# Performance work log

Measured on AMD Instinct MI355X. Metric: run time of the kernel, lower is better.

The kernel has to match this reference:

```python
import jax, jax.numpy as jnp
import numpy as np

N_NODES = 50000
N_EDGES = 1_600_000
HID = 64
BN_EPS = 1e-5


def setup_inputs() -> dict:
    key = jax.random.key(0)
    ks = jax.random.split(key, 16)
    x = jax.random.normal(ks[0], (N_NODES, 1), dtype=jnp.float32)
    edge_index = jax.random.randint(ks[1], (2, N_EDGES), 0, N_NODES, dtype=jnp.int32)
    s = 1.0 / np.sqrt(HID)
    # layer 1: 1 -> 64 -> 64
    w1a = jax.random.normal(ks[2], (1, HID), dtype=jnp.float32)
    b1a = jnp.zeros((HID,), jnp.float32)
    w2a = jax.random.normal(ks[3], (HID, HID), dtype=jnp.float32) * s
    b2a = jnp.zeros((HID,), jnp.float32)
    # layers 2-4 stacked: 64 -> 64 -> 64
    w1s = jax.random.normal(ks[4], (3, HID, HID), dtype=jnp.float32) * s
    b1s = jnp.zeros((3, HID), jnp.float32)
    w2s = jax.random.normal(ks[5], (3, HID, HID), dtype=jnp.float32) * s
    b2s = jnp.zeros((3, HID), jnp.float32)
    eps = jnp.zeros((4,), jnp.float32)  # train_eps=True, init 0
    gammas = jnp.ones((4, HID), jnp.float32)
    betas = jnp.zeros((4, HID), jnp.float32)
    fc_w = jax.random.normal(ks[6], (HID, 1), dtype=jnp.float32) * s
    fc_b = jnp.zeros((1,), jnp.float32)
    return {"x": x, "edge_index": edge_index, "w1a": w1a, "b1a": b1a,
            "w2a": w2a, "b2a": b2a, "w1s": w1s, "b1s": b1s, "w2s": w2s,
            "b2s": b2s, "eps": eps, "gammas": gammas, "betas": betas,
            "fc_w": fc_w, "fc_b": fc_b}


def _gin(h, src, dst, e, w1, b1, w2, b2):
    # sum_{j in N(i)} h_j  (messages from src, aggregated at dst)
    agg = jax.ops.segment_sum(h[src], dst, num_segments=N_NODES)
    z = (1.0 + e) * h + agg
    return jax.nn.relu(z @ w1 + b1) @ w2 + b2


def _bn(h, g, b):
    # BatchNorm1d, training mode: biased batch statistics over nodes
    mu = jnp.mean(h, axis=0)
    var = jnp.mean((h - mu) ** 2, axis=0)
    return (h - mu) * jax.lax.rsqrt(var + BN_EPS) * g + b


def reference(x, edge_index, w1a, b1a, w2a, b2a, w1s, b1s, w2s, b2s,
              eps, gammas, betas, fc_w, fc_b):
    src, dst = edge_index[0], edge_index[1]
    h = _bn(jax.nn.relu(_gin(x, src, dst, eps[0], w1a, b1a, w2a, b2a)),
            gammas[0], betas[0])
    for i in range(3):
        h = _bn(jax.nn.relu(_gin(h, src, dst, eps[i + 1],
                                 w1s[i], b1s[i], w2s[i], b2s[i])),
                gammas[i + 1], betas[i + 1])
    return h @ fc_w + fc_b
```

## Files before the change

kernel.cpp:

```cpp
#include <hip/hip_runtime.h>

#define HID 64
#define BN_EPS 1e-5f
#define WINSH 8
#define WINSZ 256
#define B1 256
#define PIT 72

typedef short bf16x8 __attribute__((ext_vector_type(8)));
typedef float f32x4 __attribute__((ext_vector_type(4)));

__device__ __forceinline__ unsigned short f2b(float f) {
    unsigned int u = __float_as_uint(f);
    u = (u + 0x7FFF + ((u >> 16) & 1)) >> 16;
    return (unsigned short)u;
}
__device__ __forceinline__ float b2f(unsigned short h) {
    return __uint_as_float(((unsigned int)h) << 16);
}
__device__ __forceinline__ f32x4 mfma_bf16(bf16x8 a, bf16x8 b, f32x4 c) {
    return __builtin_amdgcn_mfma_f32_16x16x32_bf16(a, b, c, 0, 0, 0);
}

__global__ __launch_bounds__(256) void p1_count_kernel(const int* __restrict__ dst,
                                                       int* __restrict__ cnt,
                                                       int E, int nw, int chunk) {
    __shared__ int c[256];
    int tid = threadIdx.x, b = blockIdx.x;
    c[tid] = 0;
    __syncthreads();
    int lo = b * chunk;
    int hi = lo + chunk; if (hi > E) hi = E;
    for (int e = lo + tid; e < hi; e += 256) atomicAdd(&c[dst[e] >> WINSH], 1);
    __syncthreads();
    if (tid < nw) cnt[tid * B1 + b] = c[tid];
}

__global__ __launch_bounds__(256) void scan_a_kernel(const int* __restrict__ in,
                                                     int* __restrict__ partial,
                                                     int* __restrict__ blocksum, int n) {
    __shared__ int sums[256];
    int tid = threadIdx.x;
    int i = blockIdx.x * 256 + tid;
    int v = (i < n) ? in[i] : 0;
    sums[tid] = v;
    __syncthreads();
    for (int off = 1; off < 256; off <<= 1) {
        int t = (tid >= off) ? sums[tid - off] : 0;
        __syncthreads();
        sums[tid] += t;
        __syncthreads();
    }
    if (i < n) partial[i] = sums[tid] - v;
    if (tid == 255) blocksum[blockIdx.x] = sums[255];
}

__global__ __launch_bounds__(256) void scan_b_kernel(const int* __restrict__ blocksum,
                                                     int* __restrict__ blockoff, int nb) {
    __shared__ int s[256];
    __shared__ int carry;
    int tid = threadIdx.x;
    if (tid == 0) carry = 0;
    __syncthreads();
    for (int base = 0; base < nb; base += 256) {
        int i = base + tid;
        int v = (i < nb) ? blocksum[i] : 0;
        s[tid] = v;
        __syncthreads();
        for (int off = 1; off < 256; off <<= 1) {
            int t = (tid >= off) ? s[tid - off] : 0;
            __syncthreads();
            s[tid] += t;
            __syncthreads();
        }
        if (i < nb) blockoff[i] = carry + s[tid] - v;
        __syncthreads();
        if (tid == 0) carry += s[255];
        __syncthreads();
    }
}

__global__ __launch_bounds__(256) void scan_c_kernel(const int* __restrict__ partial,
                                                     const int* __restrict__ blockoff,
                                                     int* __restrict__ outp, int n) {
    int i = blockIdx.x * 256 + threadIdx.x;
    if (i < n) outp[i] = partial[i] + blockoff[blockIdx.x];
}

__global__ __launch_bounds__(256) void p3_bucket_kernel(const int* __restrict__ src,
                                                        const int* __restrict__ dst,
                                                        const int* __restrict__ coff,
                                                        int* __restrict__ ebuf,
                                                        int E, int nw, int chunk) {
    __shared__ int cur[256];
    int tid = threadIdx.x, b = blockIdx.x;
    if (tid < nw) cur[tid] = coff[tid * B1 + b];
    __syncthreads();
    int lo = b * chunk;
    int hi = lo + chunk; if (hi > E) hi = E;
    for (int e = lo + tid; e < hi; e += 256) {
        int d = dst[e];
        int w = d >> WINSH;
        int pos = atomicAdd(&cur[w], 1);
        ebuf[pos] = src[e] | ((d & (WINSZ - 1)) << 24);
    }
}

__global__ __launch_bounds__(256) void p4_fine_kernel(const int* __restrict__ ebuf,
                                                      const int* __restrict__ coff,
                                                      int* __restrict__ csr_src,
                                                      int* __restrict__ rowptr,
                                                      int* __restrict__ deg,
                                                      int E, int n, int nw) {
    __shared__ int fcnt[256];
    __shared__ int foff[256];
    int tid = threadIdx.x, w = blockIdx.x;
    int lo = coff[w * B1];
    int hi = (w + 1 < nw) ? coff[(w + 1) * B1] : E;
    fcnt[tid] = 0;
    __syncthreads();
    for (int e = lo + tid; e < hi; e += 256) atomicAdd(&fcnt[(unsigned)ebuf[e] >> 24], 1);
    __syncthreads();
    int v = fcnt[tid];
    foff[tid] = v;
    __syncthreads();
    for (int off = 1; off < 256; off <<= 1) {
        int t = (tid >= off) ? foff[tid - off] : 0;
        __syncthreads();
        foff[tid] += t;
        __syncthreads();
    }
    int myoff = lo + foff[tid] - v;
    int node = w * WINSZ + tid;
    if (node < n) { rowptr[node] = myoff; deg[node] = v; }
    __syncthreads();
    fcnt[tid] = myoff;
    __syncthreads();
    for (int e = lo + tid; e < hi; e += 256) {
        int p = ebuf[e];
        int pos = atomicAdd(&fcnt[(unsigned)p >> 24], 1);
        csr_src[pos] = p & 0xFFFFFF;
    }
}

__global__ __launch_bounds__(256) void wprep_kernel(const float* __restrict__ w2a,
                                                    const float* __restrict__ w1s,
                                                    const float* __restrict__ w2s,
                                                    unsigned short* __restrict__ whi,
                                                    unsigned short* __restrict__ wlo) {
    int b = blockIdx.x;
    const float* srcm = (b == 0) ? w2a : (b <= 3 ? w1s + (size_t)(b - 1) * 4096
                                                 : w2s + (size_t)(b - 4) * 4096);
    unsigned short* dh = whi + (size_t)b * 4096;
    unsigned short* dl = wlo + (size_t)b * 4096;
    for (int idx = threadIdx.x; idx < 4096; idx += 256) {
        int j = idx & 7;
        int lane = (idx >> 3) & 63;
        int ntkh = idx >> 9;
        int nt = ntkh >> 1, kh = ntkh & 1;
        int nc = nt * 16 + (lane & 15);
        int k = kh * 32 + (lane >> 4) * 8 + j;
        float v = srcm[k * 64 + nc];
        unsigned short h = f2b(v);
        dh[idx] = h;
        dl[idx] = f2b(v - b2f(h));
    }
}

__global__ __launch_bounds__(256) void gather1_kernel(const float* __restrict__ x,
                                                      const int* __restrict__ rowptr,
                                                      const int* __restrict__ deg,
                                                      const int* __restrict__ csr_src,
                                                      const float* __restrict__ eps,
                                                      float* __restrict__ zscalar, int n) {
    int node = blockIdx.x * 4 + (threadIdx.x >> 6);
    int lane = threadIdx.x & 63;
    if (node >= n) return;
    int start = __builtin_amdgcn_readfirstlane(rowptr[node]);
    int cnt   = __builtin_amdgcn_readfirstlane(deg[node]);
    float a = 0.f;
    for (int i = lane; i < cnt; i += 64) a += x[csr_src[start + i]];
    for (int off = 32; off > 0; off >>= 1) a += __shfl_xor(a, off);
    if (lane == 0) zscalar[node] = (1.0f + eps[0]) * x[node] + a;
}

__global__ __launch_bounds__(256) void gatherz_kernel(const float* __restrict__ hpre,
                                                      const float* __restrict__ bnp,
                                                      const int* __restrict__ rowptr,
                                                      const int* __restrict__ deg,
                                                      const int* __restrict__ csr_src,
                                                      const float* __restrict__ eps,
                                                      int layer,
                                                      float* __restrict__ zbuf, int n) {
    int node = blockIdx.x * 4 + (threadIdx.x >> 6);
    int lane = threadIdx.x & 63;
    if (node >= n) return;
    int start = __builtin_amdgcn_readfirstlane(rowptr[node]);
    int cnt   = __builtin_amdgcn_readfirstlane(deg[node]);
    float a0 = 0.f, a1 = 0.f, a2 = 0.f, a3 = 0.f;
    float a4 = 0.f, a5 = 0.f, a6 = 0.f, a7 = 0.f;
    int e = 0;
    for (; e + 8 <= cnt; e += 8) {
        int s0 = csr_src[start + e + 0];
        int s1 = csr_src[start + e + 1];
        int s2 = csr_src[start + e + 2];
        int s3 = csr_src[start + e + 3];
        int s4 = csr_src[start + e + 4];
        int s5 = csr_src[start + e + 5];
        int s6 = csr_src[start + e + 6];
        int s7 = csr_src[start + e + 7];
        a0 += hpre[(size_t)s0 * HID + lane];
        a1 += hpre[(size_t)s1 * HID + lane];
        a2 += hpre[(size_t)s2 * HID + lane];
        a3 += hpre[(size_t)s3 * HID + lane];
        a4 += hpre[(size_t)s4 * HID + lane];
        a5 += hpre[(size_t)s5 * HID + lane];
        a6 += hpre[(size_t)s6 * HID + lane];
        a7 += hpre[(size_t)s7 * HID + lane];
    }
    for (; e < cnt; ++e) a0 += hpre[(size_t)csr_src[start + e] * HID + lane];
    float sum = ((a0 + a1) + (a2 + a3)) + ((a4 + a5) + (a6 + a7));
    float ep = 1.0f + eps[layer];
    float sc = bnp[lane], sh = bnp[64 + lane];
    float self = hpre[(size_t)node * HID + lane];
    zbuf[(size_t)node * HID + lane] =
        fmaf(sc, fmaf(ep, self, sum), sh * (ep + (float)cnt));
}

__global__ __launch_bounds__(256) void mlp_kernel(const float* __restrict__ zin,
                                                  const float* __restrict__ zscalar,
                                                  const float* __restrict__ w1a,
                                                  const float* __restrict__ b1a,
                                                  const unsigned short* __restrict__ w1h,
                                                  const unsigned short* __restrict__ w1l,
                                                  const float* __restrict__ b1v,
                                                  const unsigned short* __restrict__ w2h,
                                                  const unsigned short* __restrict__ w2l,
                                                  const float* __restrict__ b2v,
                                                  float* __restrict__ hpre,
                                                  float* __restrict__ stats,
                                                  int n, int mode) {
    __shared__ __align__(16) unsigned short Ah[64 * PIT];
    __shared__ __align__(16) unsigned short Al[64 * PIT];
    __shared__ float ssum[64], ssq[64];

    int tid = threadIdx.x;
    int base = blockIdx.x * 64;

    if (mode) {
        for (int i = tid; i < 4096; i += 256) {
            int nn = i >> 6, k = i & 63;
            float v = zin[(size_t)(base + nn) * HID + k];
            unsigned short h = f2b(v);
            Ah[nn * PIT + k] = h;
            Al[nn * PIT + k] = f2b(v - b2f(h));
        }
    } else {
        for (int i = tid; i < 4096; i += 256) {
            int nn = i >> 6, k = i & 63;
            float zv = zscalar[base + nn];
            float v = fmaxf(fmaf(zv, w1a[k], b1a[k]), 0.f);
            unsigned short h = f2b(v);
            Ah[nn * PIT + k] = h;
            Al[nn * PIT + k] = f2b(v - b2f(h));
        }
    }
    if (tid < 64) { ssum[tid] = 0.f; ssq[tid] = 0.f; }
    __syncthreads();

    int l = tid & 63;
    int m = l & 15;
    int q = l >> 4;
    int m0 = (tid >> 6) * 16;

    const bf16x8* a0h = (const bf16x8*)&Ah[(m0 + m) * PIT + q * 8];
    const bf16x8* a1h = (const bf16x8*)&Ah[(m0 + m) * PIT + 32 + q * 8];
    const bf16x8* a0l = (const bf16x8*)&Al[(m0 + m) * PIT + q * 8];
    const bf16x8* a1l = (const bf16x8*)&Al[(m0 + m) * PIT + 32 + q * 8];

    if (mode) {
        bf16x8 xa0h = *a0h, xa1h = *a1h, xa0l = *a0l, xa1l = *a1l;
        f32x4 acc[4];
#pragma unroll
        for (int nt = 0; nt < 4; ++nt) {
            size_t fo0 = ((size_t)(nt * 2 + 0) * 64 + l) * 8;
            size_t fo1 = ((size_t)(nt * 2 + 1) * 64 + l) * 8;
            bf16x8 b0h = *(const bf16x8*)(w1h + fo0);
            bf16x8 b1h_ = *(const bf16x8*)(w1h + fo1);
            bf16x8 b0l = *(const bf16x8*)(w1l + fo0);
            bf16x8 b1l_ = *(const bf16x8*)(w1l + fo1);
            f32x4 c = {0.f, 0.f, 0.f, 0.f};
            c = mfma_bf16(xa0h, b0h, c);
            c = mfma_bf16(xa0h, b0l, c);
            c = mfma_bf16(xa0l, b0h, c);
            c = mfma_bf16(xa1h, b1h_, c);
            c = mfma_bf16(xa1h, b1l_, c);
            c = mfma_bf16(xa1l, b1h_, c);
            acc[nt] = c;
        }
#pragma unroll
        for (int nt = 0; nt < 4; ++nt) {
            int col = nt * 16 + m;
            float bv = b1v[col];
#pragma unroll
            for (int r = 0; r < 4; ++r) {
                int row = m0 + q * 4 + r;
                float T = fmaxf(acc[nt][r] + bv, 0.f);
                unsigned short h = f2b(T);
                Ah[row * PIT + col] = h;
                Al[row * PIT + col] = f2b(T - b2f(h));
            }
        }
    }
    __syncthreads();

    {
        bf16x8 xa0h = *a0h, xa1h = *a1h, xa0l = *a0l, xa1l = *a1l;
        f32x4 acc[4];
#pragma unroll
        for (int nt = 0; nt < 4; ++nt) {
            size_t fo0 = ((size_t)(nt * 2 + 0) * 64 + l) * 8;
            size_t fo1 = ((size_t)(nt * 2 + 1) * 64 + l) * 8;
            bf16x8 b0h = *(const bf16x8*)(w2h + fo0);
            bf16x8 b1h_ = *(const bf16x8*)(w2h + fo1);
            bf16x8 b0l = *(const bf16x8*)(w2l + fo0);
            bf16x8 b1l_ = *(const bf16x8*)(w2l + fo1);
            f32x4 c = {0.f, 0.f, 0.f, 0.f};
            c = mfma_bf16(xa0h, b0h, c);
            c = mfma_bf16(xa0h, b0l, c);
            c = mfma_bf16(xa0l, b0h, c);
            c = mfma_bf16(xa1h, b1h_, c);
            c = mfma_bf16(xa1h, b1l_, c);
            c = mfma_bf16(xa1l, b1h_, c);
            acc[nt] = c;
        }
#pragma unroll
        for (int nt = 0; nt < 4; ++nt) {
            int col = nt * 16 + m;
            float bv = b2v[col];
            float cs = 0.f, cq = 0.f;
#pragma unroll
            for (int r = 0; r < 4; ++r) {
                int node = base + m0 + q * 4 + r;
                float h = fmaxf(acc[nt][r] + bv, 0.f);
                if (node < n) {
                    hpre[(size_t)node * HID + col] = h;
                    cs += h;
                    cq = fmaf(h, h, cq);
                }
            }
            cs += __shfl_xor(cs, 16); cs += __shfl_xor(cs, 32);
            cq += __shfl_xor(cq, 16); cq += __shfl_xor(cq, 32);
            if (q == 0) {
                atomicAdd(&ssum[col], cs);
                atomicAdd(&ssq[col], cq);
            }
        }
    }
    __syncthreads();
    if (tid < 64) {
        atomicAdd(&stats[tid], ssum[tid]);
        atomicAdd(&stats[64 + tid], ssq[tid]);
    }
}

__global__ __launch_bounds__(64) void bnfin_kernel(const float* __restrict__ stats,
                                                   const float* __restrict__ gamma,
                                                   const float* __restrict__ beta,
                                                   float* __restrict__ bnp, int n) {
    int f = threadIdx.x;
    float inv_n = 1.0f / (float)n;
    float mu = stats[f] * inv_n;
    float var = stats[64 + f] * inv_n - mu * mu;
    float inv = rsqrtf(var + BN_EPS);
    float sc = gamma[f] * inv;
    float sh = beta[f] - mu * sc;
    bnp[f] = sc;
    bnp[64 + f] = sh;
}

__global__ __launch_bounds__(256) void final_kernel(const float* __restrict__ hpre,
                                                    const float* __restrict__ bnp,
                                                    const float* __restrict__ fcw,
                                                    const float* __restrict__ fcb,
                                                    float* __restrict__ out, int n) {
    int wave = threadIdx.x >> 6;
    int lane = threadIdx.x & 63;
    int node = blockIdx.x * 4 + wave;
    if (node < n) {
        float v = hpre[(size_t)node * HID + lane];
        float t = fmaf(v, bnp[lane], bnp[64 + lane]) * fcw[lane];
        for (int off = 32; off > 0; off >>= 1) t += __shfl_xor(t, off);
        if (lane == 0) out[node] = t + fcb[0];
    }
}

extern "C" void kernel_launch(void* const* d_in, const int* in_sizes, int n_in,
                              void* d_out, int out_size, void* d_ws, size_t ws_size,
                              hipStream_t stream) {
    const float* x      = (const float*)d_in[0];
    const int*   ei     = (const int*)d_in[1];
    const float* w1a    = (const float*)d_in[2];
    const float* b1a    = (const float*)d_in[3];
    const float* w2a    = (const float*)d_in[4];
    const float* b2a    = (const float*)d_in[5];
    const float* w1s    = (const float*)d_in[6];
    const float* b1s    = (const float*)d_in[7];
    const float* w2s    = (const float*)d_in[8];
    const float* b2s    = (const float*)d_in[9];
    const float* eps    = (const float*)d_in[10];
    const float* gammas = (const float*)d_in[11];
    const float* betas  = (const float*)d_in[12];
    const float* fcw    = (const float*)d_in[13];
    const float* fcb    = (const float*)d_in[14];
    float* out = (float*)d_out;

    int n = in_sizes[0];
    int E = in_sizes[1] / 2;
    int npad = ((n + 63) / 64) * 64;
    int nblk = npad / 64;

    int nw = (n + WINSZ - 1) >> WINSH;
    int NWB = nw * B1;
    int chunk = (E + B1 - 1) / B1;
    int nbs2 = (NWB + 255) / 256;

    const int* src = ei;
    const int* dst = ei + E;

    char* p = (char*)d_ws;
    float* zbuf    = (float*)p; p += (size_t)npad * HID * 4;
    float* hpre    = (float*)p; p += (size_t)npad * HID * 4;
    float* zscalar = (float*)p; p += (size_t)npad * 4;
    float* stats   = (float*)p; p += 4 * 128 * 4;
    float* bnp     = (float*)p; p += 4 * 128 * 4;
    unsigned short* whi = (unsigned short*)p; p += 7 * 4096 * 2;
    unsigned short* wlo = (unsigned short*)p; p += 7 * 4096 * 2;
    int* deg     = (int*)p; p += (size_t)n * 4;
    int* rowptr  = (int*)p; p += (size_t)n * 4;
    int* csr_src = (int*)p; p += (size_t)E * 4;

    int* ebuf  = (int*)zbuf;
    int* cnt   = ebuf + E;
    int* cpart = cnt + NWB;
    int* coff  = cpart + NWB;
    int* bsum  = coff + NWB;
    int* boff  = bsum + nbs2;

    hipMemsetAsync(stats, 0, 4 * 128 * 4, stream);

    wprep_kernel<<<7, 256, 0, stream>>>(w2a, w1s, w2s, whi, wlo);
    p1_count_kernel<<<B1, 256, 0, stream>>>(dst, cnt, E, nw, chunk);
    scan_a_kernel<<<nbs2, 256, 0, stream>>>(cnt, cpart, bsum, NWB);
    scan_b_kernel<<<1, 256, 0, stream>>>(bsum, boff, nbs2);
    scan_c_kernel<<<nbs2, 256, 0, stream>>>(cpart, boff, coff, NWB);
    p3_bucket_kernel<<<B1, 256, 0, stream>>>(src, dst, coff, ebuf, E, nw, chunk);
    p4_fine_kernel<<<nw, 256, 0, stream>>>(ebuf, coff, csr_src, rowptr, deg, E, n, nw);

    gather1_kernel<<<(n + 3) / 4, 256, 0, stream>>>(x, rowptr, deg, csr_src, eps, zscalar, n);
    mlp_kernel<<<nblk, 256, 0, stream>>>(zbuf, zscalar, w1a, b1a,
                                         whi, wlo, b1a ,
                                         whi , wlo, b2a,
                                         hpre, stats, n, 0);
    bnfin_kernel<<<1, 64, 0, stream>>>(stats, gammas, betas, bnp, n);

    for (int l = 1; l <= 3; ++l) {
        gatherz_kernel<<<(n + 3) / 4, 256, 0, stream>>>(hpre, bnp + (l - 1) * 128,
                                                        rowptr, deg, csr_src, eps, l, zbuf, n);
        mlp_kernel<<<nblk, 256, 0, stream>>>(zbuf, zscalar, w1a, b1a,
                                             whi + (size_t)l * 4096,
                                             wlo + (size_t)l * 4096,
                                             b1s + (size_t)(l - 1) * HID,
                                             whi + (size_t)(3 + l) * 4096,
                                             wlo + (size_t)(3 + l) * 4096,
                                             b2s + (size_t)(l - 1) * HID,
                                             hpre, stats + l * 128, n, 1);
        bnfin_kernel<<<1, 64, 0, stream>>>(stats + l * 128, gammas + l * HID,
                                           betas + l * HID, bnp + l * 128, n);
    }
    final_kernel<<<(n + 3) / 4, 256, 0, stream>>>(hpre, bnp + 3 * 128, fcw, fcb, out, n);
}
```

Baseline: 442.1 us.

## Fuse neighbor gather and BN finalize into MLP kernel with fp16 gather copy

The per-layer gather is folded into the MLP kernel, so each block aggregates its 64 nodes straight into shared-memory bf16 hi/lo tiles and computes the BN scale and shift itself. This removes the separate gatherz and bnfin kernels and the zbuf round trip. Neighbor features are now read from an fp16 copy written by the previous MLP, which halves gather traffic but lowers aggregation precision. Several small setup kernels (weight prep, stats memset, count, scan_c) are also merged or removed to cut launch count, and the gather now runs at lower parallelism of 16 nodes per wave serially.

```diff
diff --git a/kernel.cpp b/kernel.cpp
--- a/kernel.cpp
+++ b/kernel.cpp
@@ -1,4 +1,5 @@
 #include <hip/hip_runtime.h>
+#include <hip/hip_fp16.h>
 
 #define HID 64
 #define BN_EPS 1e-5f
@@ -22,18 +23,47 @@
     return __builtin_amdgcn_mfma_f32_16x16x32_bf16(a, b, c, 0, 0, 0);
 }
 
-__global__ __launch_bounds__(256) void p1_count_kernel(const int* __restrict__ dst,
-                                                       int* __restrict__ cnt,
-                                                       int E, int nw, int chunk) {
-    __shared__ int c[256];
-    int tid = threadIdx.x, b = blockIdx.x;
-    c[tid] = 0;
-    __syncthreads();
-    int lo = b * chunk;
-    int hi = lo + chunk; if (hi > E) hi = E;
-    for (int e = lo + tid; e < hi; e += 256) atomicAdd(&c[dst[e] >> WINSH], 1);
-    __syncthreads();
-    if (tid < nw) cnt[tid * B1 + b] = c[tid];
+__global__ __launch_bounds__(256) void prep_kernel(const float* __restrict__ w2a,
+                                                   const float* __restrict__ w1s,
+                                                   const float* __restrict__ w2s,
+                                                   unsigned short* __restrict__ whi,
+                                                   unsigned short* __restrict__ wlo,
+                                                   float* __restrict__ stats,
+                                                   const int* __restrict__ dst,
+                                                   int* __restrict__ cnt,
+                                                   int E, int nw, int chunk) {
+    int blk = blockIdx.x, tid = threadIdx.x;
+    if (blk < 7) {
+        const float* srcm = (blk == 0) ? w2a : (blk <= 3 ? w1s + (size_t)(blk - 1) * 4096
+                                                         : w2s + (size_t)(blk - 4) * 4096);
+        unsigned short* dh = whi + (size_t)blk * 4096;
+        unsigned short* dl = wlo + (size_t)blk * 4096;
+        for (int idx = tid; idx < 4096; idx += 256) {
+            int j = idx & 7;
+            int lane = (idx >> 3) & 63;
+            int ntkh = idx >> 9;
+            int nt = ntkh >> 1, kh = ntkh & 1;
+            int nc = nt * 16 + (lane & 15);
+            int k = kh * 32 + (lane >> 4) * 8 + j;
+            float v = srcm[k * 64 + nc];
+            unsigned short h = f2b(v);
+            dh[idx] = h;
+            dl[idx] = f2b(v - b2f(h));
+        }
+    } else if (blk == 7) {
+        stats[tid] = 0.f;
+        stats[tid + 256] = 0.f;
+    } else {
+        __shared__ int c[256];
+        int b = blk - 8;
+        c[tid] = 0;
+        __syncthreads();
+        int lo = b * chunk;
+        int hi = lo + chunk; if (hi > E) hi = E;
+        for (int e = lo + tid; e < hi; e += 256) atomicAdd(&c[dst[e] >> WINSH], 1);
+        __syncthreads();
+        if (tid < nw) cnt[tid * B1 + b] = c[tid];
+    }
 }
 
 __global__ __launch_bounds__(256) void scan_a_kernel(const int* __restrict__ in,
@@ -80,21 +110,15 @@
     }
 }
 
-__global__ __launch_bounds__(256) void scan_c_kernel(const int* __restrict__ partial,
-                                                     const int* __restrict__ blockoff,
-                                                     int* __restrict__ outp, int n) {
-    int i = blockIdx.x * 256 + threadIdx.x;
-    if (i < n) outp[i] = partial[i] + blockoff[blockIdx.x];
-}
-
 __global__ __launch_bounds__(256) void p3_bucket_kernel(const int* __restrict__ src,
                                                         const int* __restrict__ dst,
-                                                        const int* __restrict__ coff,
+                                                        const int* __restrict__ cpart,
+                                                        const int* __restrict__ blockoff,
                                                         int* __restrict__ ebuf,
                                                         int E, int nw, int chunk) {
     __shared__ int cur[256];
     int tid = threadIdx.x, b = blockIdx.x;
-    if (tid < nw) cur[tid] = coff[tid * B1 + b];
+    if (tid < nw) cur[tid] = cpart[tid * B1 + b] + blockoff[tid];
     __syncthreads();
     int lo = b * chunk;
     int hi = lo + chunk; if (hi > E) hi = E;
@@ -107,7 +131,8 @@
 }
 
 __global__ __launch_bounds__(256) void p4_fine_kernel(const int* __restrict__ ebuf,
-                                                      const int* __restrict__ coff,
+                                                      const int* __restrict__ cpart,
+                                                      const int* __restrict__ blockoff,
                                                       int* __restrict__ csr_src,
                                                       int* __restrict__ rowptr,
                                                       int* __restrict__ deg,
@@ -115,8 +140,8 @@
     __shared__ int fcnt[256];
     __shared__ int foff[256];
     int tid = threadIdx.x, w = blockIdx.x;
-    int lo = coff[w * B1];
-    int hi = (w + 1 < nw) ? coff[(w + 1) * B1] : E;
+    int lo = cpart[w * B1] + blockoff[w];
+    int hi = (w + 1 < nw) ? cpart[(w + 1) * B1] + blockoff[w + 1] : E;
     fcnt[tid] = 0;
     __syncthreads();
     for (int e = lo + tid; e < hi; e += 256) atomicAdd(&fcnt[(unsigned)ebuf[e] >> 24], 1);
@@ -140,30 +165,6 @@
         int p = ebuf[e];
         int pos = atomicAdd(&fcnt[(unsigned)p >> 24], 1);
         csr_src[pos] = p & 0xFFFFFF;
-    }
-}
-
-__global__ __launch_bounds__(256) void wprep_kernel(const float* __restrict__ w2a,
-                                                    const float* __restrict__ w1s,
-                                                    const float* __restrict__ w2s,
-                                                    unsigned short* __restrict__ whi,
-                                                    unsigned short* __restrict__ wlo) {
-    int b = blockIdx.x;
-    const float* srcm = (b == 0) ? w2a : (b <= 3 ? w1s + (size_t)(b - 1) * 4096
-                                                 : w2s + (size_t)(b - 4) * 4096);
-    unsigned short* dh = whi + (size_t)b * 4096;
-    unsigned short* dl = wlo + (size_t)b * 4096;
-    for (int idx = threadIdx.x; idx < 4096; idx += 256) {
-        int j = idx & 7;
-        int lane = (idx >> 3) & 63;
-        int ntkh = idx >> 9;
-        int nt = ntkh >> 1, kh = ntkh & 1;
-        int nc = nt * 16 + (lane & 15);
-        int k = kh * 32 + (lane >> 4) * 8 + j;
-        float v = srcm[k * 64 + nc];
-        unsigned short h = f2b(v);
-        dh[idx] = h;
-        dl[idx] = f2b(v - b2f(h));
     }
 }
 
@@ -184,76 +185,91 @@
     if (lane == 0) zscalar[node] = (1.0f + eps[0]) * x[node] + a;
 }
 
-__global__ __launch_bounds__(256) void gatherz_kernel(const float* __restrict__ hpre,
-                                                      const float* __restrict__ bnp,
-                                                      const int* __restrict__ rowptr,
-                                                      const int* __restrict__ deg,
-                                                      const int* __restrict__ csr_src,
-                                                      const float* __restrict__ eps,
-                                                      int layer,
-                                                      float* __restrict__ zbuf, int n) {
-    int node = blockIdx.x * 4 + (threadIdx.x >> 6);
-    int lane = threadIdx.x & 63;
-    if (node >= n) return;
-    int start = __builtin_amdgcn_readfirstlane(rowptr[node]);
-    int cnt   = __builtin_amdgcn_readfirstlane(deg[node]);
-    float a0 = 0.f, a1 = 0.f, a2 = 0.f, a3 = 0.f;
-    float a4 = 0.f, a5 = 0.f, a6 = 0.f, a7 = 0.f;
-    int e = 0;
-    for (; e + 8 <= cnt; e += 8) {
-        int s0 = csr_src[start + e + 0];
-        int s1 = csr_src[start + e + 1];
-        int s2 = csr_src[start + e + 2];
-        int s3 = csr_src[start + e + 3];
-        int s4 = csr_src[start + e + 4];
-        int s5 = csr_src[start + e + 5];
-        int s6 = csr_src[start + e + 6];
-        int s7 = csr_src[start + e + 7];
-        a0 += hpre[(size_t)s0 * HID + lane];
-        a1 += hpre[(size_t)s1 * HID + lane];
-        a2 += hpre[(size_t)s2 * HID + lane];
-        a3 += hpre[(size_t)s3 * HID + lane];
-        a4 += hpre[(size_t)s4 * HID + lane];
-        a5 += hpre[(size_t)s5 * HID + lane];
-        a6 += hpre[(size_t)s6 * HID + lane];
-        a7 += hpre[(size_t)s7 * HID + lane];
-    }
-    for (; e < cnt; ++e) a0 += hpre[(size_t)csr_src[start + e] * HID + lane];
-    float sum = ((a0 + a1) + (a2 + a3)) + ((a4 + a5) + (a6 + a7));
-    float ep = 1.0f + eps[layer];
-    float sc = bnp[lane], sh = bnp[64 + lane];
-    float self = hpre[(size_t)node * HID + lane];
-    zbuf[(size_t)node * HID + lane] =
-        fmaf(sc, fmaf(ep, self, sum), sh * (ep + (float)cnt));
-}
-
-__global__ __launch_bounds__(256) void mlp_kernel(const float* __restrict__ zin,
-                                                  const float* __restrict__ zscalar,
+__global__ __launch_bounds__(256) void mlp_kernel(const float* __restrict__ zscalar,
                                                   const float* __restrict__ w1a,
                                                   const float* __restrict__ b1a,
+                                                  const float* __restrict__ hpre_in,
+                                                  const __half* __restrict__ hh_in,
+                                                  const float* __restrict__ stats_prev,
+                                                  const float* __restrict__ gamma_prev,
+                                                  const float* __restrict__ beta_prev,
+                                                  const int* __restrict__ rowptr,
+                                                  const int* __restrict__ deg,
+                                                  const int* __restrict__ csr_src,
+                                                  const float* __restrict__ eps,
+                                                  int layer,
                                                   const unsigned short* __restrict__ w1h,
                                                   const unsigned short* __restrict__ w1l,
                                                   const float* __restrict__ b1v,
                                                   const unsigned short* __restrict__ w2h,
                                                   const unsigned short* __restrict__ w2l,
                                                   const float* __restrict__ b2v,
-                                                  float* __restrict__ hpre,
+                                                  float* __restrict__ hpre_out,
+                                                  __half* __restrict__ hh_out,
                                                   float* __restrict__ stats,
-                                                  int n, int mode) {
+                                                  int n, int mode, int write_hh) {
     __shared__ __align__(16) unsigned short Ah[64 * PIT];
     __shared__ __align__(16) unsigned short Al[64 * PIT];
     __shared__ float ssum[64], ssq[64];
+    __shared__ float bsc[64], bsh[64];
 
     int tid = threadIdx.x;
     int base = blockIdx.x * 64;
+    int lane = tid & 63;
+    int wv = tid >> 6;
+
+    if (tid < 64) { ssum[tid] = 0.f; ssq[tid] = 0.f; }
 
     if (mode) {
-        for (int i = tid; i < 4096; i += 256) {
-            int nn = i >> 6, k = i & 63;
-            float v = zin[(size_t)(base + nn) * HID + k];
-            unsigned short h = f2b(v);
-            Ah[nn * PIT + k] = h;
-            Al[nn * PIT + k] = f2b(v - b2f(h));
+        if (tid < 64) {
+            float inv_n = 1.0f / (float)n;
+            float mu = stats_prev[tid] * inv_n;
+            float var = stats_prev[64 + tid] * inv_n - mu * mu;
+            float inv = rsqrtf(var + BN_EPS);
+            float sc = gamma_prev[tid] * inv;
+            bsc[tid] = sc;
+            bsh[tid] = beta_prev[tid] - mu * sc;
+        }
+        __syncthreads();
+        float ep = 1.0f + eps[layer];
+        float sc = bsc[lane], sh = bsh[lane];
+        for (int r = 0; r < 16; ++r) {
+            int node = base + wv * 16 + r;
+            float z = 0.f;
+            if (node < n) {
+                int start = __builtin_amdgcn_readfirstlane(rowptr[node]);
+                int cnt   = __builtin_amdgcn_readfirstlane(deg[node]);
+                float a0 = 0.f, a1 = 0.f, a2 = 0.f, a3 = 0.f;
+                float a4 = 0.f, a5 = 0.f, a6 = 0.f, a7 = 0.f;
+                int e = 0;
+                for (; e + 8 <= cnt; e += 8) {
+                    int s0 = csr_src[start + e + 0];
+                    int s1 = csr_src[start + e + 1];
+                    int s2 = csr_src[start + e + 2];
+                    int s3 = csr_src[start + e + 3];
+                    int s4 = csr_src[start + e + 4];
+                    int s5 = csr_src[start + e + 5];
+                    int s6 = csr_src[start + e + 6];
+                    int s7 = csr_src[start + e + 7];
+                    a0 += __half2float(hh_in[(size_t)s0 * HID + lane]);
+                    a1 += __half2float(hh_in[(size_t)s1 * HID + lane]);
+                    a2 += __half2float(hh_in[(size_t)s2 * HID + lane]);
+                    a3 += __half2float(hh_in[(size_t)s3 * HID + lane]);
+                    a4 += __half2float(hh_in[(size_t)s4 * HID + lane]);
+                    a5 += __half2float(hh_in[(size_t)s5 * HID + lane]);
+                    a6 += __half2float(hh_in[(size_t)s6 * HID + lane]);
+                    a7 += __half2float(hh_in[(size_t)s7 * HID + lane]);
+                }
+                for (; e < cnt; ++e)
+                    a0 += __half2float(hh_in[(size_t)csr_src[start + e] * HID + lane]);
+                float sum = ((a0 + a1) + (a2 + a3)) + ((a4 + a5) + (a6 + a7));
+                float self = hpre_in[(size_t)node * HID + lane];
+                z = fmaf(sc, fmaf(ep, self, sum), sh * (ep + (float)cnt));
+            }
+            unsigned short h = f2b(z);
+            int row = wv * 16 + r;
+            Ah[row * PIT + lane] = h;
+            Al[row * PIT + lane] = f2b(z - b2f(h));
         }
     } else {
         for (int i = tid; i < 4096; i += 256) {
@@ -265,13 +281,11 @@
             Al[nn * PIT + k] = f2b(v - b2f(h));
         }
     }
-    if (tid < 64) { ssum[tid] = 0.f; ssq[tid] = 0.f; }
-    __syncthreads();
-
-    int l = tid & 63;
-    int m = l & 15;
-    int q = l >> 4;
-    int m0 = (tid >> 6) * 16;
+    __syncthreads();
+
+    int m = lane & 15;
+    int q = lane >> 4;
+    int m0 = wv * 16;
 
     const bf16x8* a0h = (const bf16x8*)&Ah[(m0 + m) * PIT + q * 8];
     const bf16x8* a1h = (const bf16x8*)&Ah[(m0 + m) * PIT + 32 + q * 8];
@@ -283,8 +297,8 @@
         f32x4 acc[4];
 #pragma unroll
         for (int nt = 0; nt < 4; ++nt) {
-            size_t fo0 = ((size_t)(nt * 2 + 0) * 64 + l) * 8;
-            size_t fo1 = ((size_t)(nt * 2 + 1) * 64 + l) * 8;
+            size_t fo0 = ((size_t)(nt * 2 + 0) * 64 + lane) * 8;
+            size_t fo1 = ((size_t)(nt * 2 + 1) * 64 + lane) * 8;
             bf16x8 b0h = *(const bf16x8*)(w1h + fo0);
             bf16x8 b1h_ = *(const bf16x8*)(w1h + fo1);
             bf16x8 b0l = *(const bf16x8*)(w1l + fo0);
@@ -319,8 +333,8 @@
         f32x4 acc[4];
 #pragma unroll
         for (int nt = 0; nt < 4; ++nt) {
-            size_t fo0 = ((size_t)(nt * 2 + 0) * 64 + l) * 8;
-            size_t fo1 = ((size_t)(nt * 2 + 1) * 64 + l) * 8;
+            size_t fo0 = ((size_t)(nt * 2 + 0) * 64 + lane) * 8;
+            size_t fo1 = ((size_t)(nt * 2 + 1) * 64 + lane) * 8;
             bf16x8 b0h = *(const bf16x8*)(w2h + fo0);
             bf16x8 b1h_ = *(const bf16x8*)(w2h + fo1);
             bf16x8 b0l = *(const bf16x8*)(w2l + fo0);
@@ -344,7 +358,8 @@
                 int node = base + m0 + q * 4 + r;
                 float h = fmaxf(acc[nt][r] + bv, 0.f);
                 if (node < n) {
-                    hpre[(size_t)node * HID + col] = h;
+                    hpre_out[(size_t)node * HID + col] = h;
+                    if (write_hh) hh_out[(size_t)node * HID + col] = __float2half(h);
                     cs += h;
                     cq = fmaf(h, h, cq);
                 }
@@ -364,23 +379,10 @@
     }
 }
 
-__global__ __launch_bounds__(64) void bnfin_kernel(const float* __restrict__ stats,
-                                                   const float* __restrict__ gamma,
-                                                   const float* __restrict__ beta,
-                                                   float* __restrict__ bnp, int n) {
-    int f = threadIdx.x;
-    float inv_n = 1.0f / (float)n;
-    float mu = stats[f] * inv_n;
-    float var = stats[64 + f] * inv_n - mu * mu;
-    float inv = rsqrtf(var + BN_EPS);
-    float sc = gamma[f] * inv;
-    float sh = beta[f] - mu * sc;
-    bnp[f] = sc;
-    bnp[64 + f] = sh;
-}
-
 __global__ __launch_bounds__(256) void final_kernel(const float* __restrict__ hpre,
-                                                    const float* __restrict__ bnp,
+                                                    const float* __restrict__ stats,
+                                                    const float* __restrict__ gamma,
+                                                    const float* __restrict__ beta,
                                                     const float* __restrict__ fcw,
                                                     const float* __restrict__ fcb,
                                                     float* __restrict__ out, int n) {
@@ -388,8 +390,14 @@
     int lane = threadIdx.x & 63;
     int node = blockIdx.x * 4 + wave;
     if (node < n) {
+        float inv_n = 1.0f / (float)n;
+        float mu = stats[lane] * inv_n;
+        float var = stats[64 + lane] * inv_n - mu * mu;
+        float inv = rsqrtf(var + BN_EPS);
+        float sc = gamma[lane] * inv;
+        float sh = beta[lane] - mu * sc;
         float v = hpre[(size_t)node * HID + lane];
-        float t = fmaf(v, bnp[lane], bnp[64 + lane]) * fcw[lane];
+        float t = fmaf(v, sc, sh) * fcw[lane];
         for (int off = 32; off > 0; off >>= 1) t += __shfl_xor(t, off);
         if (lane == 0) out[node] = t + fcb[0];
     }
@@ -429,54 +437,61 @@
     const int* dst = ei + E;
 
     char* p = (char*)d_ws;
-    float* zbuf    = (float*)p; p += (size_t)npad * HID * 4;
-    float* hpre    = (float*)p; p += (size_t)npad * HID * 4;
+    float* hpreA   = (float*)p; p += (size_t)npad * HID * 4;
+    float* hpreB   = (float*)p; p += (size_t)npad * HID * 4;
+    __half* hhA    = (__half*)p; p += (size_t)npad * HID * 2;
+    __half* hhB    = (__half*)p; p += (size_t)npad * HID * 2;
     float* zscalar = (float*)p; p += (size_t)npad * 4;
     float* stats   = (float*)p; p += 4 * 128 * 4;
-    float* bnp     = (float*)p; p += 4 * 128 * 4;
     unsigned short* whi = (unsigned short*)p; p += 7 * 4096 * 2;
     unsigned short* wlo = (unsigned short*)p; p += 7 * 4096 * 2;
     int* deg     = (int*)p; p += (size_t)n * 4;
     int* rowptr  = (int*)p; p += (size_t)n * 4;
     int* csr_src = (int*)p; p += (size_t)E * 4;
 
-    int* ebuf  = (int*)zbuf;
-    int* cnt   = ebuf + E;
-    int* cpart = cnt + NWB;
-    int* coff  = cpart + NWB;
-    int* bsum  = coff + NWB;
-    int* boff  = bsum + nbs2;
-
-    hipMemsetAsync(stats, 0, 4 * 128 * 4, stream);
-
-    wprep_kernel<<<7, 256, 0, stream>>>(w2a, w1s, w2s, whi, wlo);
-    p1_count_kernel<<<B1, 256, 0, stream>>>(dst, cnt, E, nw, chunk);
+    int* ebuf     = (int*)hpreB;
+    int* cnt      = ebuf + E;
+    int* cpart    = cnt + NWB;
+    int* bsum     = cpart + NWB;
+    int* blockoff = bsum + nbs2;
+
+    prep_kernel<<<8 + B1, 256, 0, stream>>>(w2a, w1s, w2s, whi, wlo, stats,
+                                            dst, cnt, E, nw, chunk);
     scan_a_kernel<<<nbs2, 256, 0, stream>>>(cnt, cpart, bsum, NWB);
-    scan_b_kernel<<<1, 256, 0, stream>>>(bsum, boff, nbs2);
-    scan_c_kernel<<<nbs2, 256, 0, stream>>>(cpart, boff, coff, NWB);
-    p3_bucket_kernel<<<B1, 256, 0, stream>>>(src, dst, coff, ebuf, E, nw, chunk);
-    p4_fine_kernel<<<nw, 256, 0, stream>>>(ebuf, coff, csr_src, rowptr, deg, E, n, nw);
+    scan_b_kernel<<<1, 256, 0, stream>>>(bsum, blockoff, nbs2);
+    p3_bucket_kernel<<<B1, 256, 0, stream>>>(src, dst, cpart, blockoff, ebuf, E, nw, chunk);
+    p4_fine_kernel<<<nw, 256, 0, stream>>>(ebuf, cpart, blockoff, csr_src, rowptr, deg,
+                                           E, n, nw);
 
     gather1_kernel<<<(n + 3) / 4, 256, 0, stream>>>(x, rowptr, deg, csr_src, eps, zscalar, n);
-    mlp_kernel<<<nblk, 256, 0, stream>>>(zbuf, zscalar, w1a, b1a,
+    mlp_kernel<<<nblk, 256, 0, stream>>>(zscalar, w1a, b1a,
+                                         nullptr, nullptr, nullptr, nullptr, nullptr,
+                                         rowptr, deg, csr_src, eps, 0,
                                          whi, wlo, b1a ,
                                          whi , wlo, b2a,
-                                         hpre, stats, n, 0);
-    bnfin_kernel<<<1, 64, 0, stream>>>(stats, gammas, betas, bnp, n);
+                                         hpreA, hhA, stats, n, 0, 1);
 
     for (int l = 1; l <= 3; ++l) {
-        gatherz_kernel<<<(n + 3) / 4, 256, 0, stream>>>(hpre, bnp + (l - 1) * 128,
-                                                        rowptr, deg, csr_src, eps, l, zbuf, n);
-        mlp_kernel<<<nblk, 256, 0, stream>>>(zbuf, zscalar, w1a, b1a,
+        const float* hin  = (l & 1) ? hpreA : hpreB;
+        const __half* hhi = (l & 1) ? hhA : hhB;
+        float* hout  = (l & 1) ? hpreB : hpreA;
+        __half* hho  = (l & 1) ? hhB : hhA;
+        mlp_kernel<<<nblk, 256, 0, stream>>>(nullptr, nullptr, nullptr,
+                                             hin, hhi,
+                                             stats + (l - 1) * 128,
+                                             gammas + (l - 1) * HID,
+                                             betas + (l - 1) * HID,
+                                             rowptr, deg, csr_src, eps, l,
                                              whi + (size_t)l * 4096,
                                              wlo + (size_t)l * 4096,
                                              b1s + (size_t)(l - 1) * HID,
                                              whi + (size_t)(3 + l) * 4096,
                                              wlo + (size_t)(3 + l) * 4096,
                                              b2s + (size_t)(l - 1) * HID,
-                                             hpre, stats + l * 128, n, 1);
-        bnfin_kernel<<<1, 64, 0, stream>>>(stats + l * 128, gammas + l * HID,
-                                           betas + l * HID, bnp + l * 128, n);
-    }
-    final_kernel<<<(n + 3) / 4, 256, 0, stream>>>(hpre, bnp + 3 * 128, fcw, fcb, out, n);
-}
+                                             hout, hho, stats + l * 128,
+                                             n, 1, (l < 3) ? 1 : 0);
+    }
+    final_kernel<<<(n + 3) / 4, 256, 0, stream>>>(hpreB, stats + 3 * 128,
+                                                  gammas + 3 * HID, betas + 3 * HID,
+                                                  fcw, fcb, out, n);
+}
```

Result: no change. 445.0 us (+0.7%).
